# Kernel optimization log

Hardware: AMD Instinct MI355X
Metric: run time of the kernel (lower is better)

The kernel has to match this reference:

```python
import jax, jax.numpy as jnp
import numpy as np

N = 300000
N_LEVELS = 16
FPL = 2            # n_features_per_level
BASE = 16          # base_resolution
LOG2_T = 19       # log2_hashmap_size
T = 1 << LOG2_T
NEURONS = 64
ENC_DIM = N_LEVELS * FPL  # 32
PRIMES = np.array([1, 2654435761, 805459861, 3674653429], dtype=np.uint32)


def hash_encode(x4, table):
    """Multi-resolution 4D hash-grid encoding (tcnn HashGrid, per_level_scale=2).
    x4: [N,4] in [0,1]; table: [L, T, FPL]. Returns [N, L*FPL]."""
    xc = jnp.clip(x4, 0.0, 1.0)
    feats = []
    for l in range(N_LEVELS):
        scale = BASE * (2.0 ** l) - 1.0
        pos = xc * scale + 0.5
        p0 = jnp.floor(pos)
        w = pos - p0                      # [N,4] interp weights
        p0i = p0.astype(jnp.uint32)
        acc = jnp.zeros((x4.shape[0], FPL), dtype=table.dtype)
        for c in range(16):               # 16 hypercube corners
            off = np.array([(c >> d) & 1 for d in range(4)], dtype=np.uint32)
            idx = p0i + off               # [N,4] uint32
            h = ((idx[:, 0] * PRIMES[0]) ^ (idx[:, 1] * PRIMES[1])
                 ^ (idx[:, 2] * PRIMES[2]) ^ (idx[:, 3] * PRIMES[3]))
            h = (h & jnp.uint32(T - 1)).astype(jnp.int32)
            wsel = jnp.where(off.astype(bool), w, 1.0 - w)
            wc = wsel.prod(axis=1)        # [N]
            acc = acc + table[l][h] * wc[:, None]
        feats.append(acc)
    return jnp.concatenate(feats, axis=-1)


def mlp_head(x, W0, W1, W2):
    # FullyFusedMLP: 2 hidden ReLU layers, linear output, no biases
    h = jax.nn.relu(x @ W0)
    h = jax.nn.relu(h @ W1)
    return h @ W2


def setup_inputs() -> dict:
    ks = jax.random.split(jax.random.key(0), 32)
    d = {
        'xyz': jax.random.normal(ks[0], (N, 3), jnp.float32),
        'scales': jax.random.normal(ks[1], (N, 3), jnp.float32),
        'rotations': jax.random.normal(ks[2], (N, 4), jnp.float32),
        'opacity': jax.random.normal(ks[3], (N, 1), jnp.float32),
        'shs': jax.random.normal(ks[4], (N, 16, 3), jnp.float32),
        'time': jax.random.uniform(ks[5], (N, 1), jnp.float32),
        'xyz_bound_min': jnp.full((3,), -2.0, jnp.float32),
        'xyz_bound_max': jnp.full((3,), 2.0, jnp.float32),
        'hash_table': jax.random.uniform(ks[6], (N_LEVELS, T, FPL), jnp.float32, -1e-4, 1e-4),
        'W_enc0': jax.random.normal(ks[7], (ENC_DIM, NEURONS), jnp.float32) * 0.1,
        'W_enc1': jax.random.normal(ks[8], (NEURONS, NEURONS), jnp.float32) * 0.1,
    }
    outs = {'xyz': 3, 'scl': 3, 'rot': 4, 'op': 1, 'shs': 48}
    i = 9
    for name, od in outs.items():
        d[f'W_{name}0'] = jax.random.normal(ks[i], (NEURONS, NEURONS), jnp.float32) * 0.1
        d[f'W_{name}1'] = jax.random.normal(ks[i + 1], (NEURONS, NEURONS), jnp.float32) * 0.1
        d[f'W_{name}2'] = jax.random.normal(ks[i + 2], (NEURONS, od), jnp.float32) * 0.1
        i += 3
    return d


def reference(xyz, scales, rotations, opacity, shs, time,
              xyz_bound_min, xyz_bound_max, hash_table,
              W_enc0, W_enc1,
              W_xyz0, W_xyz1, W_xyz2,
              W_scl0, W_scl1, W_scl2,
              W_rot0, W_rot1, W_rot2,
              W_op0, W_op1, W_op2,
              W_shs0, W_shs1, W_shs2):
    # get_contracted_xyz runs under no_grad in the original
    contracted = jax.lax.stop_gradient(
        (xyz - xyz_bound_min) / (xyz_bound_max - xyz_bound_min))
    mask = jnp.all((contracted >= 0) & (contracted <= 1), axis=1)  # [N]
    x4 = jnp.concatenate([contracted, time], axis=-1)              # [N,4]
    enc = hash_encode(x4, hash_table)                              # [N,32]
    # enc_model network: 1 hidden layer, ReLU output activation
    hidden = jax.nn.relu(jax.nn.relu(enc @ W_enc0) @ W_enc1)       # [N,64]
    d_xyz = mlp_head(hidden, W_xyz0, W_xyz1, W_xyz2)
    d_rot = mlp_head(hidden, W_rot0, W_rot1, W_rot2)
    d_scl = mlp_head(hidden, W_scl0, W_scl1, W_scl2)
    d_op = mlp_head(hidden, W_op0, W_op1, W_op2)
    d_shs = mlp_head(hidden, W_shs0, W_shs1, W_shs2).reshape(-1, 16, 3)
    m1 = mask[:, None]
    new_xyz = jnp.where(m1, xyz + d_xyz, xyz)
    new_rot = jnp.where(m1, rotations + d_rot, rotations)
    new_scales = jnp.where(m1, scales + d_scl, scales)
    new_opacity = jnp.where(m1, opacity + d_op, opacity)
    new_shs = jnp.where(mask[:, None, None], shs + d_shs, shs)
    return (new_xyz, new_scales, new_rot, new_opacity, new_shs)
```

## Files before the change

kernel.cpp:

```cpp
#include <hip/hip_runtime.h>

#define NPTS 300000
#define LOG2T 19
#define TSIZE (1u<<LOG2T)
#define NROWS 300032u
#define BLKS_PER_LV 1172u

typedef float f32x4 __attribute__((ext_vector_type(4)));
typedef __bf16 bf16x8 __attribute__((ext_vector_type(8)));

__device__ __forceinline__ unsigned short f2bf(float f){
  unsigned u = __builtin_bit_cast(unsigned, f);
  u += 0x7fffu + ((u>>16)&1u);
  return (unsigned short)(u>>16);
}
__device__ __forceinline__ float bf_lo(unsigned v){ return __builtin_bit_cast(float, v<<16); }
__device__ __forceinline__ float bf_hi(unsigned v){ return __builtin_bit_cast(float, v&0xffff0000u); }

__device__ __forceinline__ unsigned qsel(uint4 q, unsigned i){
  unsigned lo = (i&1u) ? q.y : q.x;
  unsigned hi = (i&1u) ? q.w : q.z;
  return (i&2u) ? hi : lo;
}

__device__ __forceinline__ int tau(int k){
  return 16*(2*(k>>5) + (k&1)) + 4*((k>>3)&3) + ((k>>1)&3);
}

struct WP { const float* p[17]; };

__device__ const int LK[17]  = {32,64, 64,64,64, 64,64,64, 64,64,64, 64,64,64, 64,64,64};
__device__ const int LN[17]  = {64,64, 64,64, 3, 64,64, 3, 64,64, 4, 64,64, 1, 64,64,48};
__device__ const int LNT[17] = { 4, 4,  4, 4, 1,  4, 4, 1,  4, 4, 1,  4, 4, 1,  4, 4, 3};
__device__ const int LOFF[17]= {0,4096, 12288,20480,28672, 30720,38912,47104,
                                49152,57344,65536, 67584,75776,83968, 86016,94208,102400};

__global__ void prep_all(WP wp, unsigned short* wdst,
                         const float* __restrict__ t, unsigned* __restrict__ tdst){
  int gtid = blockIdx.x*blockDim.x + threadIdx.x;
  int gstr = blockDim.x*gridDim.x;
  if(tdst){
    int n = (16 << LOG2T) / 2;
    for(int i=gtid; i<n; i+=gstr){
      float4 f = ((const float4*)t)[i];
      uint2 o;
      o.x = (unsigned)f2bf(f.x) | ((unsigned)f2bf(f.y)<<16);
      o.y = (unsigned)f2bf(f.z) | ((unsigned)f2bf(f.w)<<16);
      ((uint2*)tdst)[i] = o;
    }
  }
  for(int layer=0; layer<17; layer++){
    const float* W = wp.p[layer];
    int K = LK[layer], Nn = LN[layer], NT = LNT[layer];
    unsigned short* d = wdst + LOFF[layer]/2;
    int nel = (K/32) * NT * 512;
    for(int i=gtid; i<nel; i += gstr){
      int j = i & 7, l = (i>>3)&63, fidx = i>>9;
      int kt = fidx / NT, nt = fidx - kt*NT;
      int k = kt*32 + ((l>>4)<<3) + j;
      if(layer != 0) k = tau(k);
      int n = nt*16 + (l&15);
      unsigned short v = 0;
      if(n < Nn) v = f2bf(W[k*Nn + n]);
      d[i] = v;
    }
  }
}

template<bool BT>
__global__ __launch_bounds__(256) void encode_lv(
    const float* __restrict__ xyz, const float* __restrict__ timep,
    const float* __restrict__ bmin, const float* __restrict__ bmax,
    const void* __restrict__ tab, unsigned* __restrict__ enc_t)
{
  unsigned bid = blockIdx.x;
  unsigned lv = bid / BLKS_PER_LV;
  unsigned p = (bid - lv*BLKS_PER_LV)*256u + threadIdx.x;
  size_t oidx = (size_t)lv*NROWS + p;
  if(p >= NPTS){ enc_t[oidx] = 0u; return; }

  float m0=bmin[0], m1=bmin[1], m2=bmin[2];
  float M0=bmax[0], M1=bmax[1], M2=bmax[2];
  float c0 = fminf(fmaxf((xyz[3*p  ]-m0)/(M0-m0),0.f),1.f);
  float c1 = fminf(fmaxf((xyz[3*p+1]-m1)/(M1-m1),0.f),1.f);
  float c2 = fminf(fmaxf((xyz[3*p+2]-m2)/(M2-m2),0.f),1.f);
  float c3 = fminf(fmaxf(timep[p],0.f),1.f);

  float sc = (float)(16<<lv) - 1.0f;
  float pos0 = c0*sc + 0.5f, pos1 = c1*sc + 0.5f;
  float pos2 = c2*sc + 0.5f, pos3 = c3*sc + 0.5f;
  float f0 = floorf(pos0), f1 = floorf(pos1), f2 = floorf(pos2), f3 = floorf(pos3);
  float w0 = pos0-f0, w1 = pos1-f1, w2 = pos2-f2, w3 = pos3-f3;
  unsigned i0 = (unsigned)f0, i1 = (unsigned)f1, i2 = (unsigned)f2, i3 = (unsigned)f3;
  unsigned hy0 = i1*2654435761u,     hy1 = hy0 + 2654435761u;
  unsigned hz0 = i2*805459861u,      hz1 = hz0 + 805459861u;
  unsigned ht0 = i3*3674653429u,     ht1 = ht0 + 3674653429u;
  float u0=1.f-w0, u1=1.f-w1, u2=1.f-w2, u3=1.f-w3;
  float a0 = 0.f, a1 = 0.f;
  if(BT){
    const unsigned* tb = (const unsigned*)tab + ((size_t)lv<<LOG2T);
    unsigned d = i0 ^ (i0 + 1u);
    unsigned rh[8], va[8], vb[8];
    #pragma unroll
    for(int cc=0;cc<8;cc++){
      unsigned r = ((cc&1)?hy1:hy0) ^ ((cc&2)?hz1:hz0) ^ ((cc&4)?ht1:ht0);
      rh[cc] = r;
      unsigned h0 = (i0 ^ r) & (TSIZE-1u);
      uint4 qd = *(const uint4*)(tb + (h0 & ~3u));
      unsigned e0 = h0 & 3u;
      va[cc] = qsel(qd, e0);
      vb[cc] = qsel(qd, e0 ^ (d & 3u));
    }
    if(d > 3u){
      unsigned i0p = i0 + 1u;
      #pragma unroll
      for(int cc=0;cc<8;cc++)
        vb[cc] = tb[(i0p ^ rh[cc]) & (TSIZE-1u)];
    }
    float wyz[4] = {u1*u2, w1*u2, u1*w2, w1*w2};
    #pragma unroll
    for(int cc=0;cc<8;cc++){
      float wr = wyz[cc&3] * ((cc&4)? w3 : u3);
      float wa = u0*wr, wb = w0*wr;
      a0 = fmaf(bf_lo(va[cc]), wa, a0);
      a1 = fmaf(bf_hi(va[cc]), wa, a1);
      a0 = fmaf(bf_lo(vb[cc]), wb, a0);
      a1 = fmaf(bf_hi(vb[cc]), wb, a1);
    }
  } else {
    unsigned hx0 = i0, hx1 = i0 + 1u;
    float wxy[4] = {u0*u1, w0*u1, u0*w1, w0*w1};
    float wzt[4] = {u2*u3, w2*u3, u2*w3, w2*w3};
    const float* tb = (const float*)tab + ((size_t)lv<<(LOG2T+1));
    float2 v[16];
    #pragma unroll
    for(int cc=0;cc<16;cc++){
      unsigned h = ((cc&1)?hx1:hx0) ^ ((cc&2)?hy1:hy0) ^ ((cc&4)?hz1:hz0) ^ ((cc&8)?ht1:ht0);
      v[cc] = *(const float2*)(tb + ((size_t)(h&(TSIZE-1u))<<1));
    }
    #pragma unroll
    for(int cc=0;cc<16;cc++){
      float wc = wxy[cc&3]*wzt[cc>>2];
      a0 = fmaf(v[cc].x, wc, a0);
      a1 = fmaf(v[cc].y, wc, a1);
    }
  }
  enc_t[oidx] = (unsigned)f2bf(a0) | ((unsigned)f2bf(a1)<<16);
}

__device__ __forceinline__ void pack_local(const f32x4* acc, bf16x8* out){
  #pragma unroll
  for(int kt=0;kt<2;kt++){
    unsigned w[4];
    #pragma unroll
    for(int t=0;t<4;t++){
      float x = fmaxf(acc[2*kt  ][t], 0.f);
      float y = fmaxf(acc[2*kt+1][t], 0.f);
      asm("v_cvt_pk_bf16_f32 %0, %1, %2" : "=v"(w[t]) : "v"(x), "v"(y));
    }
    out[kt] = __builtin_bit_cast(bf16x8, uint4{w[0],w[1],w[2],w[3]});
  }
}

template<int MT>
__device__ __forceinline__ void head_tail(const bf16x8* bh, const char* hb,
    const float* __restrict__ resid, float* __restrict__ outp, int od,
    int p, int q, int lane, float m){
  f32x4 acc[4];
  const bf16x8* w0 = (const bf16x8*)hb;
  #pragma unroll
  for(int mt=0;mt<4;mt++){
    f32x4 a = f32x4{0.f,0.f,0.f,0.f};
    #pragma unroll
    for(int kt=0;kt<2;kt++)
      a = __builtin_amdgcn_mfma_f32_16x16x32_bf16(w0[(kt*4+mt)*64+lane], bh[kt], a, 0,0,0);
    acc[mt] = a;
  }
  bf16x8 bx[2];
  pack_local(acc, bx);

  const bf16x8* w1 = (const bf16x8*)(hb + 8192);
  #pragma unroll
  for(int mt=0;mt<4;mt++){
    f32x4 a = f32x4{0.f,0.f,0.f,0.f};
    #pragma unroll
    for(int kt=0;kt<2;kt++)
      a = __builtin_amdgcn_mfma_f32_16x16x32_bf16(w1[(kt*4+mt)*64+lane], bx[kt], a, 0,0,0);
    acc[mt] = a;
  }
  bf16x8 by[2];
  pack_local(acc, by);

  const bf16x8* w2 = (const bf16x8*)(hb + 16384);
  f32x4 af[MT];
  #pragma unroll
  for(int mt=0;mt<MT;mt++){
    f32x4 a = f32x4{0.f,0.f,0.f,0.f};
    #pragma unroll
    for(int kt=0;kt<2;kt++)
      a = __builtin_amdgcn_mfma_f32_16x16x32_bf16(w2[(kt*MT+mt)*64+lane], by[kt], a, 0,0,0);
    af[mt] = a;
  }
  if(p < NPTS){
    #pragma unroll
    for(int mt=0;mt<MT;mt++){
      #pragma unroll
      for(int rr=0;rr<4;rr++){
        int n = 16*mt + 4*q + rr;
        if(n < od){
          size_t idx = (size_t)p*od + n;
          outp[idx] = resid[idx] + m*af[mt][rr];
        }
      }
    }
  }
}

__global__ __launch_bounds__(256,4) void mlp_k(
    const float* __restrict__ xyz, const float* __restrict__ scales,
    const float* __restrict__ rots, const float* __restrict__ opac,
    const float* __restrict__ shs,
    const float* __restrict__ bmin, const float* __restrict__ bmax,
    const unsigned* __restrict__ enc_t, const unsigned short* __restrict__ wsw,
    float* __restrict__ out)
{
  __shared__ __align__(16) char smem[40960];
  const int tid  = threadIdx.x;
  const int lane = tid & 63;
  const int wid  = blockIdx.x*4 + (tid>>6);
  const int pb   = wid*16;
  const int q = lane>>4, r = lane&15;
  const int p = pb + r;

  float m = 0.f;
  if(p < NPTS){
    float m0=bmin[0], m1=bmin[1], m2=bmin[2];
    float M0=bmax[0], M1=bmax[1], M2=bmax[2];
    float c0 = (xyz[3*p  ]-m0)/(M0-m0);
    float c1 = (xyz[3*p+1]-m1)/(M1-m1);
    float c2 = (xyz[3*p+2]-m2)/(M2-m2);
    m = (c0>=0.f && c0<=1.f && c1>=0.f && c1<=1.f && c2>=0.f && c2<=1.f) ? 1.f : 0.f;
  }

  const char* wsb = (const char*)wsw;
  uint4* s4 = (uint4*)smem;

  {
    const uint4* src = (const uint4*)(wsb + 0);
    #pragma unroll
    for(int i=0;i<8;i++){
      int idx = tid + 256*i;
      if(idx < 1920) s4[idx] = src[idx];
    }
  }
  __syncthreads();

  uint4 e;
  e.x = enc_t[(size_t)(4*q+0)*NROWS + p];
  e.y = enc_t[(size_t)(4*q+1)*NROWS + p];
  e.z = enc_t[(size_t)(4*q+2)*NROWS + p];
  e.w = enc_t[(size_t)(4*q+3)*NROWS + p];
  bf16x8 b0 = __builtin_bit_cast(bf16x8, e);

  f32x4 acc[4];
  const bf16x8* wf0 = (const bf16x8*)(smem + 0);
  #pragma unroll
  for(int mt=0;mt<4;mt++)
    acc[mt] = __builtin_amdgcn_mfma_f32_16x16x32_bf16(wf0[mt*64+lane], b0,
                                                      f32x4{0.f,0.f,0.f,0.f}, 0,0,0);
  bf16x8 bt[2];
  pack_local(acc, bt);

  const bf16x8* wf1 = (const bf16x8*)(smem + 4096);
  #pragma unroll
  for(int mt=0;mt<4;mt++){
    f32x4 a = f32x4{0.f,0.f,0.f,0.f};
    #pragma unroll
    for(int kt=0;kt<2;kt++)
      a = __builtin_amdgcn_mfma_f32_16x16x32_bf16(wf1[(kt*4+mt)*64+lane], bt[kt], a, 0,0,0);
    acc[mt] = a;
  }
  bf16x8 bh[2];
  pack_local(acc, bh);

  head_tail<1>(bh, smem+12288, xyz,    out,                 3, p,q,lane, m);
  __syncthreads();

  {
    const uint4* src = (const uint4*)(wsb + 30720);
    #pragma unroll
    for(int i=0;i<9;i++) s4[tid + 256*i] = src[tid + 256*i];
  }
  __syncthreads();
  head_tail<1>(bh, smem+0,     scales, out+(size_t)3*NPTS,  3, p,q,lane, m);
  head_tail<1>(bh, smem+18432, rots,   out+(size_t)6*NPTS,  4, p,q,lane, m);
  __syncthreads();

  {
    const uint4* src = (const uint4*)(wsb + 67584);
    #pragma unroll
    for(int i=0;i<10;i++) s4[tid + 256*i] = src[tid + 256*i];
  }
  __syncthreads();
  head_tail<1>(bh, smem+0,     opac,   out+(size_t)10*NPTS, 1, p,q,lane, m);
  head_tail<3>(bh, smem+18432, shs,    out+(size_t)11*NPTS, 48, p,q,lane, m);
}

extern "C" void kernel_launch(void* const* d_in, const int* in_sizes, int n_in,
                              void* d_out, int out_size, void* d_ws, size_t ws_size,
                              hipStream_t stream){
  (void)in_sizes; (void)n_in; (void)out_size;
  WP wp;
  for(int i=0;i<17;i++) wp.p[i] = (const float*)d_in[9+i];
  char* ws = (char*)d_ws;
  unsigned short* wsw = (unsigned short*)ws;

  const size_t TAB_OFF   = 131072;
  const size_t TAB_BYTES = (size_t)(16u<<LOG2T) * 4;
  const size_t ENC_BYTES = (size_t)16 * NROWS * 4;
  bool bf16tab = ws_size >= TAB_OFF + TAB_BYTES + ENC_BYTES;
  size_t enc_off = bf16tab ? (TAB_OFF + TAB_BYTES) : TAB_OFF;
  unsigned* encp = (unsigned*)(ws + enc_off);

  const float* table = (const float*)d_in[8];
  unsigned* tabp = bf16tab ? (unsigned*)(ws + TAB_OFF) : nullptr;

  prep_all<<<4160,256,0,stream>>>(wp, wsw, table, tabp);

  unsigned enc_blocks = 16u * BLKS_PER_LV;
  if(bf16tab){
    encode_lv<true><<<enc_blocks,256,0,stream>>>(
        (const float*)d_in[0], (const float*)d_in[5],
        (const float*)d_in[6], (const float*)d_in[7], tabp, encp);
  } else {
    encode_lv<false><<<enc_blocks,256,0,stream>>>(
        (const float*)d_in[0], (const float*)d_in[5],
        (const float*)d_in[6], (const float*)d_in[7], table, encp);
  }

  mlp_k<<<NROWS/64, 256, 0, stream>>>(
      (const float*)d_in[0], (const float*)d_in[1], (const float*)d_in[2],
      (const float*)d_in[3], (const float*)d_in[4],
      (const float*)d_in[6], (const float*)d_in[7],
      encp, wsw, (float*)d_out);
}
```

Measured before the change: 287.1 us.

## Process two 16-point tiles per wave in MLP kernel to amortize weight staging

Each wave in the fused MLP kernel now handles 32 points as two 16-point tiles, A and B. Each staged weight chunk in shared memory is reused for both tiles, and the grid is halved. This cuts the per-point cost of global-to-LDS weight copies and barriers, and exposes more independent MFMA work. The trade-off is higher register pressure, which may spill or lower occupancy under the 256x4 launch bounds.

```diff
diff --git a/kernel.cpp b/kernel.cpp
--- a/kernel.cpp
+++ b/kernel.cpp
@@ -162,6 +162,37 @@
   }
 }
 
+__device__ __forceinline__ void stem(const unsigned* __restrict__ enc_t,
+                                     const char* smem, int p, int lane, int q,
+                                     bf16x8* bh){
+  uint4 e;
+  e.x = enc_t[(size_t)(4*q+0)*NROWS + p];
+  e.y = enc_t[(size_t)(4*q+1)*NROWS + p];
+  e.z = enc_t[(size_t)(4*q+2)*NROWS + p];
+  e.w = enc_t[(size_t)(4*q+3)*NROWS + p];
+  bf16x8 b0 = __builtin_bit_cast(bf16x8, e);
+
+  f32x4 acc[4];
+  const bf16x8* wf0 = (const bf16x8*)(smem + 0);
+  #pragma unroll
+  for(int mt=0;mt<4;mt++)
+    acc[mt] = __builtin_amdgcn_mfma_f32_16x16x32_bf16(wf0[mt*64+lane], b0,
+                                                      f32x4{0.f,0.f,0.f,0.f}, 0,0,0);
+  bf16x8 bt[2];
+  pack_local(acc, bt);
+
+  const bf16x8* wf1 = (const bf16x8*)(smem + 4096);
+  #pragma unroll
+  for(int mt=0;mt<4;mt++){
+    f32x4 a = f32x4{0.f,0.f,0.f,0.f};
+    #pragma unroll
+    for(int kt=0;kt<2;kt++)
+      a = __builtin_amdgcn_mfma_f32_16x16x32_bf16(wf1[(kt*4+mt)*64+lane], bt[kt], a, 0,0,0);
+    acc[mt] = a;
+  }
+  pack_local(acc, bh);
+}
+
 template<int MT>
 __device__ __forceinline__ void head_tail(const bf16x8* bh, const char* hb,
     const float* __restrict__ resid, float* __restrict__ outp, int od,
@@ -228,18 +259,24 @@
   const int tid  = threadIdx.x;
   const int lane = tid & 63;
   const int wid  = blockIdx.x*4 + (tid>>6);
-  const int pb   = wid*16;
+  const int pb   = wid*32;
   const int q = lane>>4, r = lane&15;
-  const int p = pb + r;
-
-  float m = 0.f;
-  if(p < NPTS){
-    float m0=bmin[0], m1=bmin[1], m2=bmin[2];
-    float M0=bmax[0], M1=bmax[1], M2=bmax[2];
-    float c0 = (xyz[3*p  ]-m0)/(M0-m0);
-    float c1 = (xyz[3*p+1]-m1)/(M1-m1);
-    float c2 = (xyz[3*p+2]-m2)/(M2-m2);
-    m = (c0>=0.f && c0<=1.f && c1>=0.f && c1<=1.f && c2>=0.f && c2<=1.f) ? 1.f : 0.f;
+  const int pA = pb + r, pB = pb + 16 + r;
+
+  float m0=bmin[0], m1=bmin[1], m2=bmin[2];
+  float M0=bmax[0], M1=bmax[1], M2=bmax[2];
+  float mA = 0.f, mB = 0.f;
+  if(pA < NPTS){
+    float c0 = (xyz[3*pA  ]-m0)/(M0-m0);
+    float c1 = (xyz[3*pA+1]-m1)/(M1-m1);
+    float c2 = (xyz[3*pA+2]-m2)/(M2-m2);
+    mA = (c0>=0.f && c0<=1.f && c1>=0.f && c1<=1.f && c2>=0.f && c2<=1.f) ? 1.f : 0.f;
+  }
+  if(pB < NPTS){
+    float c0 = (xyz[3*pB  ]-m0)/(M0-m0);
+    float c1 = (xyz[3*pB+1]-m1)/(M1-m1);
+    float c2 = (xyz[3*pB+2]-m2)/(M2-m2);
+    mB = (c0>=0.f && c0<=1.f && c1>=0.f && c1<=1.f && c2>=0.f && c2<=1.f) ? 1.f : 0.f;
   }
 
   const char* wsb = (const char*)wsw;
@@ -255,35 +292,12 @@
   }
   __syncthreads();
 
-  uint4 e;
-  e.x = enc_t[(size_t)(4*q+0)*NROWS + p];
-  e.y = enc_t[(size_t)(4*q+1)*NROWS + p];
-  e.z = enc_t[(size_t)(4*q+2)*NROWS + p];
-  e.w = enc_t[(size_t)(4*q+3)*NROWS + p];
-  bf16x8 b0 = __builtin_bit_cast(bf16x8, e);
-
-  f32x4 acc[4];
-  const bf16x8* wf0 = (const bf16x8*)(smem + 0);
-  #pragma unroll
-  for(int mt=0;mt<4;mt++)
-    acc[mt] = __builtin_amdgcn_mfma_f32_16x16x32_bf16(wf0[mt*64+lane], b0,
-                                                      f32x4{0.f,0.f,0.f,0.f}, 0,0,0);
-  bf16x8 bt[2];
-  pack_local(acc, bt);
-
-  const bf16x8* wf1 = (const bf16x8*)(smem + 4096);
-  #pragma unroll
-  for(int mt=0;mt<4;mt++){
-    f32x4 a = f32x4{0.f,0.f,0.f,0.f};
-    #pragma unroll
-    for(int kt=0;kt<2;kt++)
-      a = __builtin_amdgcn_mfma_f32_16x16x32_bf16(wf1[(kt*4+mt)*64+lane], bt[kt], a, 0,0,0);
-    acc[mt] = a;
-  }
-  bf16x8 bh[2];
-  pack_local(acc, bh);
-
-  head_tail<1>(bh, smem+12288, xyz,    out,                 3, p,q,lane, m);
+  bf16x8 bhA[2], bhB[2];
+  stem(enc_t, smem, pA, lane, q, bhA);
+  stem(enc_t, smem, pB, lane, q, bhB);
+
+  head_tail<1>(bhA, smem+12288, xyz,    out,                 3, pA,q,lane, mA);
+  head_tail<1>(bhB, smem+12288, xyz,    out,                 3, pB,q,lane, mB);
   __syncthreads();
 
   {
@@ -292,8 +306,10 @@
     for(int i=0;i<9;i++) s4[tid + 256*i] = src[tid + 256*i];
   }
   __syncthreads();
-  head_tail<1>(bh, smem+0,     scales, out+(size_t)3*NPTS,  3, p,q,lane, m);
-  head_tail<1>(bh, smem+18432, rots,   out+(size_t)6*NPTS,  4, p,q,lane, m);
+  head_tail<1>(bhA, smem+0,     scales, out+(size_t)3*NPTS,  3, pA,q,lane, mA);
+  head_tail<1>(bhB, smem+0,     scales, out+(size_t)3*NPTS,  3, pB,q,lane, mB);
+  head_tail<1>(bhA, smem+18432, rots,   out+(size_t)6*NPTS,  4, pA,q,lane, mA);
+  head_tail<1>(bhB, smem+18432, rots,   out+(size_t)6*NPTS,  4, pB,q,lane, mB);
   __syncthreads();
 
   {
@@ -302,8 +318,10 @@
     for(int i=0;i<10;i++) s4[tid + 256*i] = src[tid + 256*i];
   }
   __syncthreads();
-  head_tail<1>(bh, smem+0,     opac,   out+(size_t)10*NPTS, 1, p,q,lane, m);
-  head_tail<3>(bh, smem+18432, shs,    out+(size_t)11*NPTS, 48, p,q,lane, m);
+  head_tail<1>(bhA, smem+0,     opac,   out+(size_t)10*NPTS, 1, pA,q,lane, mA);
+  head_tail<1>(bhB, smem+0,     opac,   out+(size_t)10*NPTS, 1, pB,q,lane, mB);
+  head_tail<3>(bhA, smem+18432, shs,    out+(size_t)11*NPTS, 48, pA,q,lane, mA);
+  head_tail<3>(bhB, smem+18432, shs,    out+(size_t)11*NPTS, 48, pB,q,lane, mB);
 }
 
 extern "C" void kernel_launch(void* const* d_in, const int* in_sizes, int n_in,
@@ -338,7 +356,7 @@
         (const float*)d_in[6], (const float*)d_in[7], table, encp);
   }
 
-  mlp_k<<<NROWS/64, 256, 0, stream>>>(
+  mlp_k<<<NROWS/128, 256, 0, stream>>>(
       (const float*)d_in[0], (const float*)d_in[1], (const float*)d_in[2],
       (const float*)d_in[3], (const float*)d_in[4],
       (const float*)d_in[6], (const float*)d_in[7],
```

New measurement: 280.5 us, median of 2. -2.3%, faster.

## Process four 16-point tiles per wave to amortize LDS weight staging

Applied to the files above, without the earlier changes.

Each wave in the MLP kernel now handles 64 points as four 16-point sub-tiles instead of one, and the grid shrinks fourfold to match. Every block still stages all head weights through shared memory in three phases, but that staging and its barriers are now spread over four times as many points. In exchange, each thread keeps four sets of hidden activations and masks live, which raises register pressure. With fewer blocks there is also less parallelism to hide latency.

```diff
diff --git a/kernel.cpp b/kernel.cpp
--- a/kernel.cpp
+++ b/kernel.cpp
@@ -162,6 +162,37 @@
   }
 }
 
+__device__ __forceinline__ void stem(const unsigned* __restrict__ enc_t,
+                                     const char* smem, int p, int lane, int q,
+                                     bf16x8* bh){
+  uint4 e;
+  e.x = enc_t[(size_t)(4*q+0)*NROWS + p];
+  e.y = enc_t[(size_t)(4*q+1)*NROWS + p];
+  e.z = enc_t[(size_t)(4*q+2)*NROWS + p];
+  e.w = enc_t[(size_t)(4*q+3)*NROWS + p];
+  bf16x8 b0 = __builtin_bit_cast(bf16x8, e);
+
+  f32x4 acc[4];
+  const bf16x8* wf0 = (const bf16x8*)(smem + 0);
+  #pragma unroll
+  for(int mt=0;mt<4;mt++)
+    acc[mt] = __builtin_amdgcn_mfma_f32_16x16x32_bf16(wf0[mt*64+lane], b0,
+                                                      f32x4{0.f,0.f,0.f,0.f}, 0,0,0);
+  bf16x8 bt[2];
+  pack_local(acc, bt);
+
+  const bf16x8* wf1 = (const bf16x8*)(smem + 4096);
+  #pragma unroll
+  for(int mt=0;mt<4;mt++){
+    f32x4 a = f32x4{0.f,0.f,0.f,0.f};
+    #pragma unroll
+    for(int kt=0;kt<2;kt++)
+      a = __builtin_amdgcn_mfma_f32_16x16x32_bf16(wf1[(kt*4+mt)*64+lane], bt[kt], a, 0,0,0);
+    acc[mt] = a;
+  }
+  pack_local(acc, bh);
+}
+
 template<int MT>
 __device__ __forceinline__ void head_tail(const bf16x8* bh, const char* hb,
     const float* __restrict__ resid, float* __restrict__ outp, int od,
@@ -228,18 +259,25 @@
   const int tid  = threadIdx.x;
   const int lane = tid & 63;
   const int wid  = blockIdx.x*4 + (tid>>6);
-  const int pb   = wid*16;
+  const int pb   = wid*64;
   const int q = lane>>4, r = lane&15;
-  const int p = pb + r;
-
-  float m = 0.f;
-  if(p < NPTS){
-    float m0=bmin[0], m1=bmin[1], m2=bmin[2];
-    float M0=bmax[0], M1=bmax[1], M2=bmax[2];
-    float c0 = (xyz[3*p  ]-m0)/(M0-m0);
-    float c1 = (xyz[3*p+1]-m1)/(M1-m1);
-    float c2 = (xyz[3*p+2]-m2)/(M2-m2);
-    m = (c0>=0.f && c0<=1.f && c1>=0.f && c1<=1.f && c2>=0.f && c2<=1.f) ? 1.f : 0.f;
+
+  float m0=bmin[0], m1=bmin[1], m2=bmin[2];
+  float M0=bmax[0], M1=bmax[1], M2=bmax[2];
+  int   pp[4];
+  float mm[4];
+  #pragma unroll
+  for(int b=0;b<4;b++){
+    int p = pb + 16*b + r;
+    pp[b] = p;
+    float m = 0.f;
+    if(p < NPTS){
+      float c0 = (xyz[3*p  ]-m0)/(M0-m0);
+      float c1 = (xyz[3*p+1]-m1)/(M1-m1);
+      float c2 = (xyz[3*p+2]-m2)/(M2-m2);
+      m = (c0>=0.f && c0<=1.f && c1>=0.f && c1<=1.f && c2>=0.f && c2<=1.f) ? 1.f : 0.f;
+    }
+    mm[b] = m;
   }
 
   const char* wsb = (const char*)wsw;
@@ -255,35 +293,14 @@
   }
   __syncthreads();
 
-  uint4 e;
-  e.x = enc_t[(size_t)(4*q+0)*NROWS + p];
-  e.y = enc_t[(size_t)(4*q+1)*NROWS + p];
-  e.z = enc_t[(size_t)(4*q+2)*NROWS + p];
-  e.w = enc_t[(size_t)(4*q+3)*NROWS + p];
-  bf16x8 b0 = __builtin_bit_cast(bf16x8, e);
-
-  f32x4 acc[4];
-  const bf16x8* wf0 = (const bf16x8*)(smem + 0);
-  #pragma unroll
-  for(int mt=0;mt<4;mt++)
-    acc[mt] = __builtin_amdgcn_mfma_f32_16x16x32_bf16(wf0[mt*64+lane], b0,
-                                                      f32x4{0.f,0.f,0.f,0.f}, 0,0,0);
-  bf16x8 bt[2];
-  pack_local(acc, bt);
-
-  const bf16x8* wf1 = (const bf16x8*)(smem + 4096);
-  #pragma unroll
-  for(int mt=0;mt<4;mt++){
-    f32x4 a = f32x4{0.f,0.f,0.f,0.f};
-    #pragma unroll
-    for(int kt=0;kt<2;kt++)
-      a = __builtin_amdgcn_mfma_f32_16x16x32_bf16(wf1[(kt*4+mt)*64+lane], bt[kt], a, 0,0,0);
-    acc[mt] = a;
-  }
-  bf16x8 bh[2];
-  pack_local(acc, bh);
-
-  head_tail<1>(bh, smem+12288, xyz,    out,                 3, p,q,lane, m);
+  bf16x8 bh[4][2];
+  #pragma unroll
+  for(int b=0;b<4;b++)
+    stem(enc_t, smem, pp[b], lane, q, bh[b]);
+
+  #pragma unroll
+  for(int b=0;b<4;b++)
+    head_tail<1>(bh[b], smem+12288, xyz, out, 3, pp[b], q, lane, mm[b]);
   __syncthreads();
 
   {
@@ -292,8 +309,12 @@
     for(int i=0;i<9;i++) s4[tid + 256*i] = src[tid + 256*i];
   }
   __syncthreads();
-  head_tail<1>(bh, smem+0,     scales, out+(size_t)3*NPTS,  3, p,q,lane, m);
-  head_tail<1>(bh, smem+18432, rots,   out+(size_t)6*NPTS,  4, p,q,lane, m);
+  #pragma unroll
+  for(int b=0;b<4;b++)
+    head_tail<1>(bh[b], smem+0,     scales, out+(size_t)3*NPTS, 3, pp[b], q, lane, mm[b]);
+  #pragma unroll
+  for(int b=0;b<4;b++)
+    head_tail<1>(bh[b], smem+18432, rots,   out+(size_t)6*NPTS, 4, pp[b], q, lane, mm[b]);
   __syncthreads();
 
   {
@@ -302,8 +323,12 @@
     for(int i=0;i<10;i++) s4[tid + 256*i] = src[tid + 256*i];
   }
   __syncthreads();
-  head_tail<1>(bh, smem+0,     opac,   out+(size_t)10*NPTS, 1, p,q,lane, m);
-  head_tail<3>(bh, smem+18432, shs,    out+(size_t)11*NPTS, 48, p,q,lane, m);
+  #pragma unroll
+  for(int b=0;b<4;b++)
+    head_tail<1>(bh[b], smem+0,     opac,   out+(size_t)10*NPTS, 1,  pp[b], q, lane, mm[b]);
+  #pragma unroll
+  for(int b=0;b<4;b++)
+    head_tail<3>(bh[b], smem+18432, shs,    out+(size_t)11*NPTS, 48, pp[b], q, lane, mm[b]);
 }
 
 extern "C" void kernel_launch(void* const* d_in, const int* in_sizes, int n_in,
@@ -338,7 +363,7 @@
         (const float*)d_in[6], (const float*)d_in[7], table, encp);
   }
 
-  mlp_k<<<NROWS/64, 256, 0, stream>>>(
+  mlp_k<<<NROWS/256, 256, 0, stream>>>(
       (const float*)d_in[0], (const float*)d_in[1], (const float*)d_in[2],
       (const float*)d_in[3], (const float*)d_in[4],
       (const float*)d_in[6], (const float*)d_in[7],
```

Measured after the change: 310.2 us. +8.0%, slower.
